# Kernel tuning notes

Measured on AMD Instinct MI355X. Metric: run time of the kernel, lower is better.

The kernel has to match this reference:

```python
import jax, jax.numpy as jnp
import numpy as np
import math

B, N, D, H, BS = 1, 2048, 1024, 16, 256  # batch, seq, d_model, heads, block_size


def setup_inputs() -> dict:
    key = jax.random.key(0)
    ks = jax.random.split(key, 8)
    s = 0.02  # init scale for projection weights
    return {
        "x": jax.random.normal(ks[0], (B, N, D), jnp.float32),
        "distance_bias": jax.random.uniform(ks[1], (N, N), dtype=jnp.float32),
        "Wq": jax.random.normal(ks[2], (D, D), jnp.float32) * s,
        "bq": jnp.zeros((D,), jnp.float32),
        "Wk": jax.random.normal(ks[3], (D, D), jnp.float32) * s,
        "bk": jnp.zeros((D,), jnp.float32),
        "Wv": jax.random.normal(ks[4], (D, D), jnp.float32) * s,
        "bv": jnp.zeros((D,), jnp.float32),
        "Wo": jax.random.normal(ks[5], (D, D), jnp.float32) * s,
        "bo": jnp.zeros((D,), jnp.float32),
    }


def reference(x, distance_bias, Wq, bq, Wk, bk, Wv, bv, Wo, bo):
    Bm, Nm, Dm = x.shape
    dk = Dm // H
    scale = 1.0 / math.sqrt(dk)
    nb = Nm // BS  # number of blocks along sequence

    def proj(W, b):
        # torch Linear: x @ W.T + b, then split heads -> [B, H, N, dk]
        return (x @ W.T + b).reshape(Bm, Nm, H, dk).transpose(0, 2, 1, 3)

    Q, K, V = proj(Wq, bq), proj(Wk, bk), proj(Wv, bv)

    # scores with toroidal bias subtracted (matches `scores - bias_block`)
    scores = jnp.einsum('bhqd,bhkd->bhqk', Q, K) * scale - distance_bias[None, None]
    # view as [B, H, n_qblk, BS, n_kblk, BS] and softmax PER (q-block, k-block)
    s6 = scores.reshape(Bm, H, nb, BS, nb, BS)
    w = jax.nn.softmax(s6, axis=-1)  # softmax over keys within each kv block

    Vb = V.reshape(Bm, H, nb, BS, dk)
    # sum over all kv blocks of (per-block softmax) @ V_block
    num = jnp.einsum('bhqsnk,bhnkd->bhqsd', w, Vb)  # [B,H,nb,BS,dk]
    # accumulated normalizer = sum of per-block softmax weights over all kv blocks
    norm = jnp.sum(w, axis=(4, 5))  # [B,H,nb,BS]
    O = num / (norm[..., None] + 1e-8)

    O = O.reshape(Bm, H, Nm, dk).transpose(0, 2, 1, 3).reshape(Bm, Nm, Dm)
    return O @ Wo.T + bo
```

## Files before the change

kernel.cpp:

```cpp
#include <hip/hip_runtime.h>
#include <hip/hip_fp16.h>

typedef _Float16 half8 __attribute__((ext_vector_type(8)));
typedef _Float16 half4v __attribute__((ext_vector_type(4)));
typedef float f32x4 __attribute__((ext_vector_type(4)));

#define NSEQ 2048
#define DMOD 1024
#define NHEAD 16
#define DK 64

#define GLOAD_LDS16(gp, lp) __builtin_amdgcn_global_load_lds(                 \
    (const __attribute__((address_space(1))) void*)(gp),                      \
    (__attribute__((address_space(3))) void*)(lp), 16, 0, 0)

#define WAIT_VM(n) (0xF70 | (n))


__global__ __launch_bounds__(256) void cast_pack(
    const float* __restrict__ x, const float* __restrict__ wq,
    const float* __restrict__ wk, const float* __restrict__ wv,
    const float* __restrict__ wo, _Float16* __restrict__ dst)
{
    const int w = blockIdx.x * 4 + (threadIdx.x >> 6);
    const int ln = threadIdx.x & 63, m = ln & 15, qd = ln >> 4;
    const float* src; _Float16* d; int loc;
    if (w < 4096) { src = x; d = dst; loc = w; }
    else {
        const int w2 = w - 4096, mat = w2 >> 11;
        loc = w2 & 2047;
        src = mat == 0 ? wq : mat == 1 ? wk : mat == 2 ? wv : wo;
        d = dst + 2097152 + mat * 1048576;
    }
    const int st = loc >> 5, kc = loc & 31;
    const float* p = src + (size_t)(st * 16 + m) * 1024 + kc * 32 + qd * 8;
    float4 a = *(const float4*)p, b = *(const float4*)(p + 4);
    half8 h;
    h[0] = (_Float16)a.x; h[1] = (_Float16)a.y; h[2] = (_Float16)a.z; h[3] = (_Float16)a.w;
    h[4] = (_Float16)b.x; h[5] = (_Float16)b.y; h[6] = (_Float16)b.z; h[7] = (_Float16)b.w;
    *(half8*)(d + (size_t)(loc * 64 + ln) * 8) = h;
}

__global__ __launch_bounds__(256) void cvt_bias(
    const float* __restrict__ src, _Float16* __restrict__ dst)
{
    int i = (blockIdx.x * 256 + threadIdx.x) * 4;
    float4 v = *(const float4*)(src + i);
    half4v h;
    h[0] = (_Float16)v.x; h[1] = (_Float16)v.y;
    h[2] = (_Float16)v.z; h[3] = (_Float16)v.w;
    *(half4v*)(dst + i) = h;
}

__global__ __launch_bounds__(256) void combine(
    const _Float16* __restrict__ a, const _Float16* __restrict__ b,
    _Float16* __restrict__ o)
{
    int i = (blockIdx.x * 256 + threadIdx.x) * 8;
    half8 x = *(const half8*)(a + i);
    half8 y = *(const half8*)(b + i);
    half8 r;
#pragma unroll
    for (int j = 0; j < 8; ++j) r[j] = (_Float16)((float)x[j] + (float)y[j]);
    *(half8*)(o + i) = r;
}

template<int BM, int BN, int MODE>
__global__ __launch_bounds__(256) void tgemm(
    const _Float16* __restrict__ A,
    const _Float16* __restrict__ W0, const _Float16* __restrict__ W1,
    const _Float16* __restrict__ W2,
    const float* __restrict__ b0, const float* __restrict__ b1,
    const float* __restrict__ b2,
    _Float16* __restrict__ oQ, _Float16* __restrict__ oK,
    _Float16* __restrict__ oV, float* __restrict__ oF)
{
    constexpr int MT = BM / 32, NT = BN / 32;
    constexpr int NA = BM / 64, NB = BN / 64;
    __shared__ _Float16 sA[3 * BM * 32];
    __shared__ _Float16 sB[3 * BN * 32];
    const int tid = threadIdx.x, wv = tid >> 6, ln = tid & 63;
    const int m = ln & 15, qd = ln >> 4;
    const int row0 = blockIdx.x * BM;

    int sel = 0, colbase;
    const _Float16* W; const float* bias;
    if constexpr (MODE == 0) {
        sel = blockIdx.y >> 3;
        colbase = (blockIdx.y & 7) * BN;
        W = sel == 0 ? W0 : sel == 1 ? W1 : W2;
        bias = sel == 0 ? b0 : sel == 1 ? b1 : b2;
    } else {
        colbase = blockIdx.y * BN;
        W = W0; bias = b0;
    }
    const int wr = wv >> 1, wc = wv & 1;

    f32x4 acc[MT][NT];
#pragma unroll
    for (int i = 0; i < MT; ++i)
#pragma unroll
        for (int j = 0; j < NT; ++j) acc[i][j] = (f32x4){0.f, 0.f, 0.f, 0.f};

    auto stage = [&](int kc, int b) {
        _Float16* dA = sA + b * (BM * 32);
        _Float16* dB = sB + b * (BN * 32);
#pragma unroll
        for (int ra = 0; ra < NA; ++ra) {
            const int st = ra * 4 + wv;
            GLOAD_LDS16(A + ((size_t)((row0 >> 4) + st) * 32 + kc) * 512 + ln * 8,
                        dA + st * 512);
        }
#pragma unroll
        for (int rb = 0; rb < NB; ++rb) {
            const int st = rb * 4 + wv;
            GLOAD_LDS16(W + ((size_t)((colbase >> 4) + st) * 32 + kc) * 512 + ln * 8,
                        dB + st * 512);
        }
    };
    auto step = [&](int b) {
        const _Float16* cA = sA + b * (BM * 32);
        const _Float16* cB = sB + b * (BN * 32);
        half8 af[MT], bf[NT];
#pragma unroll
        for (int i = 0; i < MT; ++i)
            af[i] = *(const half8*)(cA + ((wr * MT + i) * 64 + ln) * 8);
#pragma unroll
        for (int j = 0; j < NT; ++j)
            bf[j] = *(const half8*)(cB + ((wc * NT + j) * 64 + ln) * 8);
#pragma unroll
        for (int i = 0; i < MT; ++i)
#pragma unroll
            for (int j = 0; j < NT; ++j)
                acc[i][j] = __builtin_amdgcn_mfma_f32_16x16x32_f16(af[i], bf[j], acc[i][j], 0, 0, 0);
    };

    stage(0, 0);
    stage(1, 1);
#pragma unroll
    for (int kc = 0; kc < 31; ++kc) {
        __builtin_amdgcn_s_waitcnt(WAIT_VM(NA + NB));
        __builtin_amdgcn_s_barrier();
        if (kc < 30) stage(kc + 2, (kc + 2) % 3);
        step(kc % 3);
    }
    __builtin_amdgcn_s_waitcnt(WAIT_VM(0));
    __builtin_amdgcn_s_barrier();
    step(1);

#pragma unroll
    for (int j = 0; j < NT; ++j) {
        const int col = colbase + wc * (BN / 2) + j * 16 + m;
        const float bv = bias[col];
#pragma unroll
        for (int i = 0; i < MT; ++i) {
            const int crow0 = row0 + wr * (BM / 2) + i * 16 + qd * 4;
            if constexpr (MODE == 1) {
#pragma unroll
                for (int r = 0; r < 4; ++r)
                    oF[(size_t)(crow0 + r) * DMOD + col] = acc[i][j][r] + bv;
            } else {
                const int h = col >> 6, d = col & 63;
                if (sel == 0) {
#pragma unroll
                    for (int r = 0; r < 4; ++r)
                        oQ[h * (NSEQ * DK) + (crow0 + r) * DK + d] =
                            (_Float16)((acc[i][j][r] + bv) * 0.125f);
                } else if (sel == 1) {
#pragma unroll
                    for (int r = 0; r < 4; ++r) {
                        const int n = crow0 + r;
                        oK[(size_t)(((h * 16 + (n >> 7)) * 16
                                     + ((n >> 4) & 7) * 2 + (d >> 5)) * 64
                                    + (n & 15) + 16 * ((d >> 3) & 3)) * 8
                           + (d & 7)] = (_Float16)(acc[i][j][r] + bv);
                    }
                } else {
                    half4v hv;
#pragma unroll
                    for (int r = 0; r < 4; ++r) hv[r] = (_Float16)(acc[i][j][r] + bv);
                    const int n0 = crow0;
                    *(half4v*)(oV + (size_t)(((h * 16 + (n0 >> 7)) * 16
                                              + ((n0 >> 5) & 3) * 4 + ((d >> 4) & 3)) * 64
                                             + (d & 15) + 16 * ((n0 >> 3) & 3)) * 8
                               + (n0 & 7)) = hv;
                }
            }
        }
    }
}

__global__ __launch_bounds__(512, 4) void attn(
    const _Float16* __restrict__ Q, const _Float16* __restrict__ Kt,
    const _Float16* __restrict__ Vt, const _Float16* __restrict__ bias_h,
    _Float16* __restrict__ Op)
{
    __shared__ _Float16 sK[8192];
    __shared__ _Float16 sV[8192];
    __shared__ _Float16 sP[16384];
    const int tid = threadIdx.x, wv = tid >> 6, ln = tid & 63;
    const int m = ln & 15, qd = ln >> 4;
    const int h = blockIdx.x;
    const int q0 = blockIdx.y * 128 + wv * 16;
    const int kvb = blockIdx.z * 8;
    const _Float16* Qh = Q + h * (NSEQ * DK);
    const _Float16* Kh = Kt + h * (NSEQ * DK) + kvb * 8192;
    const _Float16* Vh = Vt + h * (NSEQ * DK) + kvb * 8192;
    const _Float16* brow = bias_h + (size_t)(q0 + m) * NSEQ + kvb * 128;

    half8 qf[2];
    qf[0] = *(const half8*)(Qh + (q0 + m) * DK + qd * 8);
    qf[1] = *(const half8*)(Qh + (q0 + m) * DK + 32 + qd * 8);

    f32x4 oacc[4], oU[4];
#pragma unroll
    for (int v = 0; v < 4; ++v) {
        oacc[v] = (f32x4){0.f, 0.f, 0.f, 0.f};
        oU[v]   = (f32x4){0.f, 0.f, 0.f, 0.f};
    }
    float bsum = 0.f;

    for (int ls = 0; ls < 8; ++ls) {
        if (ls) __syncthreads();
        GLOAD_LDS16(Kh + ls * 8192 + wv * 512 + ln * 8, sK + wv * 512);
        GLOAD_LDS16(Kh + ls * 8192 + (wv + 8) * 512 + ln * 8, sK + (wv + 8) * 512);
        GLOAD_LDS16(Vh + ls * 8192 + wv * 512 + ln * 8, sV + wv * 512);
        GLOAD_LDS16(Vh + ls * 8192 + (wv + 8) * 512 + ln * 8, sV + (wv + 8) * 512);
        half4v bcur[8];
#pragma unroll
        for (int t = 0; t < 8; ++t)
            bcur[t] = *(const half4v*)(brow + ls * 128 + t * 16 + qd * 4);
        __syncthreads();

#pragma unroll
        for (int t = 0; t < 8; ++t) {
            half8 kf0 = *(const half8*)(sK + ((t * 2 + 0) * 64 + ln) * 8);
            half8 kf1 = *(const half8*)(sK + ((t * 2 + 1) * 64 + ln) * 8);
            f32x4 s = {0.f, 0.f, 0.f, 0.f};
            s = __builtin_amdgcn_mfma_f32_16x16x32_f16(kf0, qf[0], s, 0, 0, 0);
            s = __builtin_amdgcn_mfma_f32_16x16x32_f16(kf1, qf[1], s, 0, 0, 0);
            float p0 = __expf(s[0] - (float)bcur[t][0]);
            float p1 = __expf(s[1] - (float)bcur[t][1]);
            float p2 = __expf(s[2] - (float)bcur[t][2]);
            float p3 = __expf(s[3] - (float)bcur[t][3]);
            bsum += (p0 + p1) + (p2 + p3);
            half4v ph;
            ph[0] = (_Float16)p0; ph[1] = (_Float16)p1;
            ph[2] = (_Float16)p2; ph[3] = (_Float16)p3;
            *(half4v*)(sP + wv * 2048 + (t >> 1) * 512
                       + (((t & 1) * 2 + (qd >> 1)) * 16 + m) * 8
                       + (qd & 1) * 4) = ph;
        }

#pragma unroll
        for (int kk = 0; kk < 4; ++kk) {
            half8 pa = *(const half8*)(sP + wv * 2048 + kk * 512 + ln * 8);
#pragma unroll
            for (int vt = 0; vt < 4; ++vt) {
                half8 vb = *(const half8*)(sV + ((kk * 4 + vt) * 64 + ln) * 8);
                oU[vt] = __builtin_amdgcn_mfma_f32_16x16x32_f16(pa, vb, oU[vt], 0, 0, 0);
            }
        }

        if (ls & 1) {
            float s2 = bsum;
            s2 += __shfl_xor(s2, 16, 64);
            s2 += __shfl_xor(s2, 32, 64);
            float inv = 1.0f / (8.0f * s2);
            float iv[4];
#pragma unroll
            for (int r = 0; r < 4; ++r) iv[r] = __shfl(inv, qd * 4 + r, 64);
#pragma unroll
            for (int vt = 0; vt < 4; ++vt) {
#pragma unroll
                for (int r = 0; r < 4; ++r) oacc[vt][r] += iv[r] * oU[vt][r];
                oU[vt] = (f32x4){0.f, 0.f, 0.f, 0.f};
            }
            bsum = 0.f;
        }
    }

    _Float16* Opz = Op + (size_t)blockIdx.z * 2097152;
    const int st = blockIdx.y * 8 + wv;
#pragma unroll
    for (int vt = 0; vt < 4; ++vt) {
        const int d = h * 64 + vt * 16 + m;
        _Float16* base = Opz + (size_t)(st * 32 + (d >> 5)) * 512
                         + ((d >> 3) & 3) * 128 + (d & 7);
#pragma unroll
        for (int r = 0; r < 4; ++r)
            base[(qd * 4 + r) * 8] = (_Float16)oacc[vt][r];
    }
}

extern "C" void kernel_launch(void* const* d_in, const int* in_sizes, int n_in,
                              void* d_out, int out_size, void* d_ws, size_t ws_size,
                              hipStream_t stream)
{
    const float* x  = (const float*)d_in[0];
    const float* db = (const float*)d_in[1];
    const float* Wq = (const float*)d_in[2];
    const float* bq = (const float*)d_in[3];
    const float* Wk = (const float*)d_in[4];
    const float* bk = (const float*)d_in[5];
    const float* Wv = (const float*)d_in[6];
    const float* bv = (const float*)d_in[7];
    const float* Wo = (const float*)d_in[8];
    const float* bo = (const float*)d_in[9];
    float* out = (float*)d_out;

    _Float16* ws  = (_Float16*)d_ws;
    _Float16* xh  = ws;
    _Float16* wqh = xh  + 2097152;
    _Float16* wkh = wqh + 1048576;
    _Float16* wvh = wkh + 1048576;
    _Float16* woh = wvh + 1048576;
    _Float16* Qb  = woh + 1048576;
    _Float16* Kb  = Qb  + 2097152;
    _Float16* Vtb = Kb  + 2097152;
    _Float16* Oh0 = Vtb + 2097152;
    _Float16* Oh1 = Oh0 + 2097152;
    _Float16* bh  = ws;

    cast_pack<<<3072, 256, 0, stream>>>(x, Wq, Wk, Wv, Wo, xh);

    tgemm<128, 128, 0><<<dim3(16, 24), 256, 0, stream>>>(
        xh, wqh, wkh, wvh, bq, bk, bv, Qb, Kb, Vtb, nullptr);

    cvt_bias<<<4096, 256, 0, stream>>>(db, bh);

    attn<<<dim3(NHEAD, NSEQ / 128, 2), 512, 0, stream>>>(Qb, Kb, Vtb, bh, Oh0);

    combine<<<1024, 256, 0, stream>>>(Oh0, Oh1, Oh0);

    tgemm<64, 128, 1><<<dim3(32, 8), 256, 0, stream>>>(
        Oh0, woh, nullptr, nullptr, bo, nullptr, nullptr,
        nullptr, nullptr, nullptr, out);
}
```

Measured before the change: 185.3 us.

## Keep softmax probabilities in registers and stage full 256-key blocks per step

The P tile no longer goes through shared memory. The exp results are packed straight into the A operand of a 16x16x16 MFMA, and V is read from LDS in a layout that matches that operand, so the sP write/read round trip and its LDS traffic go away. Each loop step now loads a whole 256-key block of K and V (4 steps instead of 8), and the second half of the bias row is loaded mid-loop. This doubles the K/V LDS footprint, uses a narrower MFMA shape with twice as many instructions for P·V, and keeps more bias values live in registers. Together these may lower occupancy.

```diff
diff --git a/kernel.cpp b/kernel.cpp
--- a/kernel.cpp
+++ b/kernel.cpp
@@ -195,74 +195,77 @@
     const _Float16* __restrict__ Vt, const _Float16* __restrict__ bias_h,
     _Float16* __restrict__ Op)
 {
-    __shared__ _Float16 sK[8192];
-    __shared__ _Float16 sV[8192];
-    __shared__ _Float16 sP[16384];
+    __shared__ _Float16 sK[16384];
+    __shared__ _Float16 sV[16384];
     const int tid = threadIdx.x, wv = tid >> 6, ln = tid & 63;
     const int m = ln & 15, qd = ln >> 4;
     const int h = blockIdx.x;
     const int q0 = blockIdx.y * 128 + wv * 16;
-    const int kvb = blockIdx.z * 8;
     const _Float16* Qh = Q + h * (NSEQ * DK);
-    const _Float16* Kh = Kt + h * (NSEQ * DK) + kvb * 8192;
-    const _Float16* Vh = Vt + h * (NSEQ * DK) + kvb * 8192;
-    const _Float16* brow = bias_h + (size_t)(q0 + m) * NSEQ + kvb * 128;
+    const _Float16* Kh = Kt + h * (NSEQ * DK) + (size_t)blockIdx.z * 65536;
+    const _Float16* Vh = Vt + h * (NSEQ * DK) + (size_t)blockIdx.z * 65536;
+    const _Float16* brow = bias_h + (size_t)(q0 + m) * NSEQ + blockIdx.z * 1024;
 
     half8 qf[2];
     qf[0] = *(const half8*)(Qh + (q0 + m) * DK + qd * 8);
     qf[1] = *(const half8*)(Qh + (q0 + m) * DK + 32 + qd * 8);
 
-    f32x4 oacc[4], oU[4];
-#pragma unroll
-    for (int v = 0; v < 4; ++v) {
-        oacc[v] = (f32x4){0.f, 0.f, 0.f, 0.f};
-        oU[v]   = (f32x4){0.f, 0.f, 0.f, 0.f};
-    }
-    float bsum = 0.f;
-
-    for (int ls = 0; ls < 8; ++ls) {
+    const int vofE = (m + 16 * (qd >> 1)) * 8 + (qd & 1) * 4;
+    const int vofO = vofE + 256;
+
+    f32x4 oacc[4];
+#pragma unroll
+    for (int v = 0; v < 4; ++v) oacc[v] = (f32x4){0.f, 0.f, 0.f, 0.f};
+
+    for (int ls = 0; ls < 4; ++ls) {
         if (ls) __syncthreads();
-        GLOAD_LDS16(Kh + ls * 8192 + wv * 512 + ln * 8, sK + wv * 512);
-        GLOAD_LDS16(Kh + ls * 8192 + (wv + 8) * 512 + ln * 8, sK + (wv + 8) * 512);
-        GLOAD_LDS16(Vh + ls * 8192 + wv * 512 + ln * 8, sV + wv * 512);
-        GLOAD_LDS16(Vh + ls * 8192 + (wv + 8) * 512 + ln * 8, sV + (wv + 8) * 512);
-        half4v bcur[8];
+#pragma unroll
+        for (int j = 0; j < 4; ++j) {
+            const int f = j * 8 + wv;
+            GLOAD_LDS16(Kh + ls * 16384 + f * 512 + ln * 8, sK + f * 512);
+            GLOAD_LDS16(Vh + ls * 16384 + f * 512 + ln * 8, sV + f * 512);
+        }
+        half4v bc0[8], bc1[8];
 #pragma unroll
         for (int t = 0; t < 8; ++t)
-            bcur[t] = *(const half4v*)(brow + ls * 128 + t * 16 + qd * 4);
+            bc0[t] = *(const half4v*)(brow + ls * 256 + t * 16 + qd * 4);
         __syncthreads();
 
-#pragma unroll
-        for (int t = 0; t < 8; ++t) {
+        f32x4 oU[4];
+#pragma unroll
+        for (int v = 0; v < 4; ++v) oU[v] = (f32x4){0.f, 0.f, 0.f, 0.f};
+        float bsum = 0.f;
+
+#pragma unroll
+        for (int t = 0; t < 16; ++t) {
+            if (t == 4) {
+#pragma unroll
+                for (int tt = 0; tt < 8; ++tt)
+                    bc1[tt] = *(const half4v*)(brow + ls * 256 + 128 + tt * 16 + qd * 4);
+            }
             half8 kf0 = *(const half8*)(sK + ((t * 2 + 0) * 64 + ln) * 8);
             half8 kf1 = *(const half8*)(sK + ((t * 2 + 1) * 64 + ln) * 8);
             f32x4 s = {0.f, 0.f, 0.f, 0.f};
             s = __builtin_amdgcn_mfma_f32_16x16x32_f16(kf0, qf[0], s, 0, 0, 0);
             s = __builtin_amdgcn_mfma_f32_16x16x32_f16(kf1, qf[1], s, 0, 0, 0);
-            float p0 = __expf(s[0] - (float)bcur[t][0]);
-            float p1 = __expf(s[1] - (float)bcur[t][1]);
-            float p2 = __expf(s[2] - (float)bcur[t][2]);
-            float p3 = __expf(s[3] - (float)bcur[t][3]);
+            half4v bt = (t < 8) ? bc0[t] : bc1[t - 8];
+            float p0 = __expf(s[0] - (float)bt[0]);
+            float p1 = __expf(s[1] - (float)bt[1]);
+            float p2 = __expf(s[2] - (float)bt[2]);
+            float p3 = __expf(s[3] - (float)bt[3]);
             bsum += (p0 + p1) + (p2 + p3);
-            half4v ph;
-            ph[0] = (_Float16)p0; ph[1] = (_Float16)p1;
-            ph[2] = (_Float16)p2; ph[3] = (_Float16)p3;
-            *(half4v*)(sP + wv * 2048 + (t >> 1) * 512
-                       + (((t & 1) * 2 + (qd >> 1)) * 16 + m) * 8
-                       + (qd & 1) * 4) = ph;
-        }
-
-#pragma unroll
-        for (int kk = 0; kk < 4; ++kk) {
-            half8 pa = *(const half8*)(sP + wv * 2048 + kk * 512 + ln * 8);
+            half4v pa;
+            pa[0] = (_Float16)p0; pa[1] = (_Float16)p1;
+            pa[2] = (_Float16)p2; pa[3] = (_Float16)p3;
+            const _Float16* vbp = sV + (t >> 1) * 2048 + ((t & 1) ? vofO : vofE);
 #pragma unroll
             for (int vt = 0; vt < 4; ++vt) {
-                half8 vb = *(const half8*)(sV + ((kk * 4 + vt) * 64 + ln) * 8);
-                oU[vt] = __builtin_amdgcn_mfma_f32_16x16x32_f16(pa, vb, oU[vt], 0, 0, 0);
+                half4v vb = *(const half4v*)(vbp + vt * 512);
+                oU[vt] = __builtin_amdgcn_mfma_f32_16x16x16f16(pa, vb, oU[vt], 0, 0, 0);
             }
         }
 
-        if (ls & 1) {
+        {
             float s2 = bsum;
             s2 += __shfl_xor(s2, 16, 64);
             s2 += __shfl_xor(s2, 32, 64);
@@ -271,12 +274,9 @@
 #pragma unroll
             for (int r = 0; r < 4; ++r) iv[r] = __shfl(inv, qd * 4 + r, 64);
 #pragma unroll
-            for (int vt = 0; vt < 4; ++vt) {
+            for (int vt = 0; vt < 4; ++vt)
 #pragma unroll
                 for (int r = 0; r < 4; ++r) oacc[vt][r] += iv[r] * oU[vt][r];
-                oU[vt] = (f32x4){0.f, 0.f, 0.f, 0.f};
-            }
-            bsum = 0.f;
         }
     }
 
```

Measured after the change: 192.7 us. 1.04x slower.

## Double-buffer K/V staging and feed P from registers via 16x16x16 MFMA

Applied to the files above, without the earlier changes.

Double-buffers the K/V shared-memory tiles and bias registers so the next KV tile is loaded while the current one is computed, using raw barriers and vmcnt waits. It removes the sP round trip: the exponentiated scores go straight from registers into a 16x16x16 MFMA against V, and the V pack layout in the projection kernel changes to match. This cuts LDS traffic and one sync per step. The costs are twice the K/V LDS footprint, more bias registers, and twice as many smaller MFMA instructions for the PV product.

```diff
diff --git a/kernel.cpp b/kernel.cpp
--- a/kernel.cpp
+++ b/kernel.cpp
@@ -15,6 +15,8 @@
     (__attribute__((address_space(3))) void*)(lp), 16, 0, 0)
 
 #define WAIT_VM(n) (0xF70 | (n))
+
+template<bool B> struct Bc { static constexpr bool value = B; };
 
 
 __global__ __launch_bounds__(256) void cast_pack(
@@ -180,10 +182,10 @@
 #pragma unroll
                     for (int r = 0; r < 4; ++r) hv[r] = (_Float16)(acc[i][j][r] + bv);
                     const int n0 = crow0;
-                    *(half4v*)(oV + (size_t)(((h * 16 + (n0 >> 7)) * 16
-                                              + ((n0 >> 5) & 3) * 4 + ((d >> 4) & 3)) * 64
-                                             + (d & 15) + 16 * ((n0 >> 3) & 3)) * 8
-                               + (n0 & 7)) = hv;
+                    *(half4v*)(oV + (size_t)(h * 16 + (n0 >> 7)) * 8192
+                               + ((((n0 >> 4) & 7) * 4 + ((d >> 4) & 3)) * 64
+                                  + ((n0 >> 2) & 3) * 16 + (d & 15)) * 4
+                               + (n0 & 3)) = hv;
                 }
             }
         }
@@ -195,9 +197,8 @@
     const _Float16* __restrict__ Vt, const _Float16* __restrict__ bias_h,
     _Float16* __restrict__ Op)
 {
-    __shared__ _Float16 sK[8192];
-    __shared__ _Float16 sV[8192];
-    __shared__ _Float16 sP[16384];
+    __shared__ _Float16 sK[2][8192];
+    __shared__ _Float16 sV[2][8192];
     const int tid = threadIdx.x, wv = tid >> 6, ln = tid & 63;
     const int m = ln & 15, qd = ln >> 4;
     const int h = blockIdx.x;
@@ -208,9 +209,10 @@
     const _Float16* Vh = Vt + h * (NSEQ * DK) + kvb * 8192;
     const _Float16* brow = bias_h + (size_t)(q0 + m) * NSEQ + kvb * 128;
 
-    half8 qf[2];
-    qf[0] = *(const half8*)(Qh + (q0 + m) * DK + qd * 8);
-    qf[1] = *(const half8*)(Qh + (q0 + m) * DK + 32 + qd * 8);
+    half8 qf0 = *(const half8*)(Qh + (q0 + m) * DK + qd * 8);
+    half8 qf1 = *(const half8*)(Qh + (q0 + m) * DK + 32 + qd * 8);
+
+    const int voff = ln * 4;
 
     f32x4 oacc[4], oU[4];
 #pragma unroll
@@ -220,45 +222,55 @@
     }
     float bsum = 0.f;
 
-    for (int ls = 0; ls < 8; ++ls) {
-        if (ls) __syncthreads();
-        GLOAD_LDS16(Kh + ls * 8192 + wv * 512 + ln * 8, sK + wv * 512);
-        GLOAD_LDS16(Kh + ls * 8192 + (wv + 8) * 512 + ln * 8, sK + (wv + 8) * 512);
-        GLOAD_LDS16(Vh + ls * 8192 + wv * 512 + ln * 8, sV + wv * 512);
-        GLOAD_LDS16(Vh + ls * 8192 + (wv + 8) * 512 + ln * 8, sV + (wv + 8) * 512);
-        half4v bcur[8];
-#pragma unroll
-        for (int t = 0; t < 8; ++t)
-            bcur[t] = *(const half4v*)(brow + ls * 128 + t * 16 + qd * 4);
-        __syncthreads();
-
+    auto stageKV = [&](int ls, int b) {
+        GLOAD_LDS16(Kh + ls * 8192 + wv * 512 + ln * 8, sK[b] + wv * 512);
+        GLOAD_LDS16(Kh + ls * 8192 + (wv + 8) * 512 + ln * 8, sK[b] + (wv + 8) * 512);
+        GLOAD_LDS16(Vh + ls * 8192 + wv * 512 + ln * 8, sV[b] + wv * 512);
+        GLOAD_LDS16(Vh + ls * 8192 + (wv + 8) * 512 + ln * 8, sV[b] + (wv + 8) * 512);
+    };
+
+    half4v bA[8], bB[8];
+    stageKV(0, 0);
+#pragma unroll
+    for (int t = 0; t < 8; ++t)
+        bA[t] = *(const half4v*)(brow + t * 16 + qd * 4);
+
+    auto step = [&](int ls, half4v (&bc)[8], half4v (&bn)[8], auto lastc) {
+        constexpr bool LAST = decltype(lastc)::value;
+        if (ls) __builtin_amdgcn_s_barrier();
+        if constexpr (!LAST) {
+            stageKV(ls + 1, (ls + 1) & 1);
+#pragma unroll
+            for (int t = 0; t < 8; ++t)
+                bn[t] = *(const half4v*)(brow + (ls + 1) * 128 + t * 16 + qd * 4);
+            __builtin_amdgcn_s_waitcnt(WAIT_VM(12));
+        } else {
+            __builtin_amdgcn_s_waitcnt(WAIT_VM(0));
+        }
+        __builtin_amdgcn_s_barrier();
+
+        const _Float16* sKc = sK[ls & 1];
+        const _Float16* sVc = sV[ls & 1];
 #pragma unroll
         for (int t = 0; t < 8; ++t) {
-            half8 kf0 = *(const half8*)(sK + ((t * 2 + 0) * 64 + ln) * 8);
-            half8 kf1 = *(const half8*)(sK + ((t * 2 + 1) * 64 + ln) * 8);
+            half8 kf0 = *(const half8*)(sKc + ((t * 2 + 0) * 64 + ln) * 8);
+            half8 kf1 = *(const half8*)(sKc + ((t * 2 + 1) * 64 + ln) * 8);
             f32x4 s = {0.f, 0.f, 0.f, 0.f};
-            s = __builtin_amdgcn_mfma_f32_16x16x32_f16(kf0, qf[0], s, 0, 0, 0);
-            s = __builtin_amdgcn_mfma_f32_16x16x32_f16(kf1, qf[1], s, 0, 0, 0);
-            float p0 = __expf(s[0] - (float)bcur[t][0]);
-            float p1 = __expf(s[1] - (float)bcur[t][1]);
-            float p2 = __expf(s[2] - (float)bcur[t][2]);
-            float p3 = __expf(s[3] - (float)bcur[t][3]);
+            s = __builtin_amdgcn_mfma_f32_16x16x32_f16(kf0, qf0, s, 0, 0, 0);
+            s = __builtin_amdgcn_mfma_f32_16x16x32_f16(kf1, qf1, s, 0, 0, 0);
+            float p0 = __expf(s[0] - (float)bc[t][0]);
+            float p1 = __expf(s[1] - (float)bc[t][1]);
+            float p2 = __expf(s[2] - (float)bc[t][2]);
+            float p3 = __expf(s[3] - (float)bc[t][3]);
             bsum += (p0 + p1) + (p2 + p3);
-            half4v ph;
-            ph[0] = (_Float16)p0; ph[1] = (_Float16)p1;
-            ph[2] = (_Float16)p2; ph[3] = (_Float16)p3;
-            *(half4v*)(sP + wv * 2048 + (t >> 1) * 512
-                       + (((t & 1) * 2 + (qd >> 1)) * 16 + m) * 8
-                       + (qd & 1) * 4) = ph;
-        }
-
-#pragma unroll
-        for (int kk = 0; kk < 4; ++kk) {
-            half8 pa = *(const half8*)(sP + wv * 2048 + kk * 512 + ln * 8);
+            half4v pa;
+            pa[0] = (_Float16)p0; pa[1] = (_Float16)p1;
+            pa[2] = (_Float16)p2; pa[3] = (_Float16)p3;
+            const _Float16* vbp = sVc + t * 1024 + voff;
 #pragma unroll
             for (int vt = 0; vt < 4; ++vt) {
-                half8 vb = *(const half8*)(sV + ((kk * 4 + vt) * 64 + ln) * 8);
-                oU[vt] = __builtin_amdgcn_mfma_f32_16x16x32_f16(pa, vb, oU[vt], 0, 0, 0);
+                half4v vb = *(const half4v*)(vbp + vt * 256);
+                oU[vt] = __builtin_amdgcn_mfma_f32_16x16x16f16(pa, vb, oU[vt], 0, 0, 0);
             }
         }
 
@@ -278,7 +290,16 @@
             }
             bsum = 0.f;
         }
-    }
+    };
+
+    step(0, bA, bB, Bc<false>{});
+    step(1, bB, bA, Bc<false>{});
+    step(2, bA, bB, Bc<false>{});
+    step(3, bB, bA, Bc<false>{});
+    step(4, bA, bB, Bc<false>{});
+    step(5, bB, bA, Bc<false>{});
+    step(6, bA, bB, Bc<false>{});
+    step(7, bB, bA, Bc<true>{});
 
     _Float16* Opz = Op + (size_t)blockIdx.z * 2097152;
     const int st = blockIdx.y * 8 + wv;
```

Result: slower. 191.9 us (+3.6%).

## Read fp32 distance bias directly in attention and shrink QKV GEMM tile

Applied to the files above, without the earlier changes.

Removes the separate kernel that converted the 2048x2048 distance bias to fp16. The attention kernel now loads the fp32 bias directly, which drops one launch and a full write-then-read round trip. In exchange, each of the 16 heads reads twice as many bias bytes per tile. Separately, the QKV projection GEMM switches from 128x128 to 64x128 tiles, doubling the grid to improve CU occupancy on the 768-block launch.

```diff
diff --git a/kernel.cpp b/kernel.cpp
--- a/kernel.cpp
+++ b/kernel.cpp
@@ -39,17 +39,6 @@
     h[0] = (_Float16)a.x; h[1] = (_Float16)a.y; h[2] = (_Float16)a.z; h[3] = (_Float16)a.w;
     h[4] = (_Float16)b.x; h[5] = (_Float16)b.y; h[6] = (_Float16)b.z; h[7] = (_Float16)b.w;
     *(half8*)(d + (size_t)(loc * 64 + ln) * 8) = h;
-}
-
-__global__ __launch_bounds__(256) void cvt_bias(
-    const float* __restrict__ src, _Float16* __restrict__ dst)
-{
-    int i = (blockIdx.x * 256 + threadIdx.x) * 4;
-    float4 v = *(const float4*)(src + i);
-    half4v h;
-    h[0] = (_Float16)v.x; h[1] = (_Float16)v.y;
-    h[2] = (_Float16)v.z; h[3] = (_Float16)v.w;
-    *(half4v*)(dst + i) = h;
 }
 
 __global__ __launch_bounds__(256) void combine(
@@ -192,7 +181,7 @@
 
 __global__ __launch_bounds__(512, 4) void attn(
     const _Float16* __restrict__ Q, const _Float16* __restrict__ Kt,
-    const _Float16* __restrict__ Vt, const _Float16* __restrict__ bias_h,
+    const _Float16* __restrict__ Vt, const float* __restrict__ bias_f,
     _Float16* __restrict__ Op)
 {
     __shared__ _Float16 sK[8192];
@@ -206,7 +195,7 @@
     const _Float16* Qh = Q + h * (NSEQ * DK);
     const _Float16* Kh = Kt + h * (NSEQ * DK) + kvb * 8192;
     const _Float16* Vh = Vt + h * (NSEQ * DK) + kvb * 8192;
-    const _Float16* brow = bias_h + (size_t)(q0 + m) * NSEQ + kvb * 128;
+    const float* brow = bias_f + (size_t)(q0 + m) * NSEQ + kvb * 128;
 
     half8 qf[2];
     qf[0] = *(const half8*)(Qh + (q0 + m) * DK + qd * 8);
@@ -226,10 +215,10 @@
         GLOAD_LDS16(Kh + ls * 8192 + (wv + 8) * 512 + ln * 8, sK + (wv + 8) * 512);
         GLOAD_LDS16(Vh + ls * 8192 + wv * 512 + ln * 8, sV + wv * 512);
         GLOAD_LDS16(Vh + ls * 8192 + (wv + 8) * 512 + ln * 8, sV + (wv + 8) * 512);
-        half4v bcur[8];
+        float4 bcur[8];
 #pragma unroll
         for (int t = 0; t < 8; ++t)
-            bcur[t] = *(const half4v*)(brow + ls * 128 + t * 16 + qd * 4);
+            bcur[t] = *(const float4*)(brow + ls * 128 + t * 16 + qd * 4);
         __syncthreads();
 
 #pragma unroll
@@ -239,10 +228,10 @@
             f32x4 s = {0.f, 0.f, 0.f, 0.f};
             s = __builtin_amdgcn_mfma_f32_16x16x32_f16(kf0, qf[0], s, 0, 0, 0);
             s = __builtin_amdgcn_mfma_f32_16x16x32_f16(kf1, qf[1], s, 0, 0, 0);
-            float p0 = __expf(s[0] - (float)bcur[t][0]);
-            float p1 = __expf(s[1] - (float)bcur[t][1]);
-            float p2 = __expf(s[2] - (float)bcur[t][2]);
-            float p3 = __expf(s[3] - (float)bcur[t][3]);
+            float p0 = __expf(s[0] - bcur[t].x);
+            float p1 = __expf(s[1] - bcur[t].y);
+            float p2 = __expf(s[2] - bcur[t].z);
+            float p3 = __expf(s[3] - bcur[t].w);
             bsum += (p0 + p1) + (p2 + p3);
             half4v ph;
             ph[0] = (_Float16)p0; ph[1] = (_Float16)p1;
@@ -320,16 +309,13 @@
     _Float16* Vtb = Kb  + 2097152;
     _Float16* Oh0 = Vtb + 2097152;
     _Float16* Oh1 = Oh0 + 2097152;
-    _Float16* bh  = ws;
 
     cast_pack<<<3072, 256, 0, stream>>>(x, Wq, Wk, Wv, Wo, xh);
 
-    tgemm<128, 128, 0><<<dim3(16, 24), 256, 0, stream>>>(
+    tgemm<64, 128, 0><<<dim3(32, 24), 256, 0, stream>>>(
         xh, wqh, wkh, wvh, bq, bk, bv, Qb, Kb, Vtb, nullptr);
 
-    cvt_bias<<<4096, 256, 0, stream>>>(db, bh);
-
-    attn<<<dim3(NHEAD, NSEQ / 128, 2), 512, 0, stream>>>(Qb, Kb, Vtb, bh, Oh0);
+    attn<<<dim3(NHEAD, NSEQ / 128, 2), 512, 0, stream>>>(Qb, Kb, Vtb, db, Oh0);
 
     combine<<<1024, 256, 0, stream>>>(Oh0, Oh1, Oh0);
 
```

Measured after the change: 181.3 us. 2.2% less time.
